# Optimization experiments

Hardware: AMD Instinct MI355X
Metric: run time of the kernel (lower is better)

Reference implementation:

```python
import jax, jax.numpy as jnp
import numpy as np

B = 65536
IN = 64
H = 16
PF = 64


def _linear_params(key, out_dim, in_dim):
    k1, k2 = jax.random.split(key)
    bound = 1.0 / np.sqrt(in_dim)
    W = jax.random.uniform(k1, (out_dim, in_dim), jnp.float32, -bound, bound)
    b = jax.random.uniform(k2, (out_dim,), jnp.float32, -bound, bound)
    return W, b


def setup_inputs() -> dict:
    key = jax.random.key(0)
    ks = jax.random.split(key, 20)
    inp = {}
    for i, name in enumerate(['a', 'v', 'l', 'p_a', 'p_v', 'p_l', 'mean']):
        inp[name] = jax.random.normal(ks[i], (B, IN), jnp.float32)
    inp['Wa'], inp['ba'] = _linear_params(ks[7], H, IN)
    inp['Wv'], inp['bv'] = _linear_params(ks[8], H, IN)
    inp['Wl'], inp['bl'] = _linear_params(ks[9], H, IN)
    inp['Wap'], inp['bap'] = _linear_params(ks[10], H, IN)
    inp['Wvp'], inp['bvp'] = _linear_params(ks[11], H, IN)
    inp['Wlp'], inp['blp'] = _linear_params(ks[12], H, IN)
    inp['Wf1'], inp['bf1'] = _linear_params(ks[13], PF, H ** 3 // 16)
    inp['Wfp1'], inp['bfp1'] = _linear_params(ks[14], PF, H ** 3 // 16)
    inp['Wng'], inp['bng'] = _linear_params(ks[15], 64, 128)
    inp['rm1'] = jnp.zeros((128,), jnp.float32)  # normGate2 running_mean buffers (eval mode)
    inp['rm2'] = jnp.zeros((128,), jnp.float32)
    return inp


def _maxpool2(x):
    # 2x2 stride-2 max pool over the last two dims of [B, Hd, Wd]
    b, hd, wd = x.shape
    return x.reshape(b, hd // 2, 2, wd // 2, 2).max(axis=(2, 4))


def _trimodal_fusion(x_h, y_h, z_h):
    # outer product [B,H,H] -> pool -> [B,H*H//4,1] bmm [B,1,H] -> pool -> flatten
    f = x_h[:, :, None] * y_h[:, None, :]            # [B,16,16]
    f = _maxpool2(f)                                 # [B,8,8]
    f = f.reshape(-1, H * H // 4, 1) * z_h[:, None, :]  # [B,64,16]
    f = _maxpool2(f)                                 # [B,32,8]
    return f.reshape(x_h.shape[0], -1)               # [B,256]


def _norm_gate(x, running_mean):
    # eval-mode normGate2: y = x * sigmoid(|x - running_mean|)
    return x * jax.nn.sigmoid(jnp.abs(x - running_mean))


def reference(a, v, l, p_a, p_v, p_l, mean,
              Wa, ba, Wv, bv, Wl, bl, Wap, bap, Wvp, bvp, Wlp, blp,
              Wf1, bf1, Wfp1, bfp1, Wng, bng, rm1, rm2):
    a_h = jax.nn.sigmoid(a @ Wa.T + ba)
    v_h = jax.nn.sigmoid(v @ Wv.T + bv)
    l_h = jax.nn.sigmoid(l @ Wl.T + bl)
    fusion_1 = jax.nn.leaky_relu(_trimodal_fusion(a_h, v_h, l_h) @ Wf1.T + bf1)

    pa_h = jax.nn.sigmoid(p_a @ Wap.T + bap)
    pv_h = jax.nn.sigmoid(p_v @ Wvp.T + bvp)
    pl_h = jax.nn.sigmoid(p_l @ Wlp.T + blp)
    fusion_2 = jax.nn.leaky_relu(_trimodal_fusion(pa_h, pv_h, pl_h) @ Wfp1.T + bfp1)

    out = _norm_gate(jnp.concatenate([fusion_2, mean], axis=1), rm1)   # [B,128]
    out = out @ Wng.T + bng                                            # [B,64]
    out = _norm_gate(jnp.concatenate([out, fusion_1], axis=1), rm2)    # [B,128]
    return out
```

## Files before the change

### kernel.cpp

```cpp
#include <hip/hip_runtime.h>
#include <hip/hip_bf16.h>


typedef __attribute__((ext_vector_type(8))) short short8;
typedef __attribute__((ext_vector_type(4))) float f32x4;

#define MFMA16(A, B, C) __builtin_amdgcn_mfma_f32_16x16x32_bf16((A), (B), (C), 0, 0, 0)

#define ASM_LOAD_F4(dst, p) \
    asm volatile("global_load_dwordx4 %0, %1, off" : "=v"(dst) : "v"(p) : "memory")
#define VMWAIT(N) do { asm volatile("s_waitcnt vmcnt(" #N ")" ::: "memory"); \
                       __builtin_amdgcn_sched_barrier(0); } while (0)

__device__ __forceinline__ float fast_sigmoid(float x) {
    return __builtin_amdgcn_rcpf(1.0f + __expf(-x));
}
__device__ __forceinline__ float gate(float x, float rm) {
    return x * fast_sigmoid(fabsf(x - rm));
}
__device__ __forceinline__ float lrelu(float x) {
    return x >= 0.0f ? x : 0.01f * x;
}
__device__ __forceinline__ short f2bf(float f) {
    union { float f; unsigned u; } x; x.f = f;
    unsigned r = (x.u + 0x7FFF + ((x.u >> 16) & 1)) >> 16;
    return (short)r;
}
__device__ __forceinline__ short8 pack8(const float* xs) {
    union { short8 s; __hip_bfloat162 h[4]; } u;
    #pragma unroll
    for (int i = 0; i < 4; ++i) {
        float2 t; t.x = xs[2 * i]; t.y = xs[2 * i + 1];
        u.h[i] = __float22bfloat162_rn(t);
    }
    return u.s;
}
__device__ __forceinline__ f32x4 pmax_xor(f32x4 v, int mask) {
    f32x4 r;
    #pragma unroll
    for (int i = 0; i < 4; ++i) r[i] = fmaxf(v[i], __shfl_xor(v[i], mask, 64));
    return r;
}

__device__ __forceinline__ void dma_1k(const short* src, short* dst_lds, int lane) {
    __builtin_amdgcn_global_load_lds(
        (const __attribute__((address_space(1))) unsigned int*)(const void*)(src + lane * 8),
        (__attribute__((address_space(3))) unsigned int*)(void*)(dst_lds),
        16, 0, 0);
}

__device__ __forceinline__ void proj_mfma2r(const f32x4* in,
                                            const short8* __restrict__ wfr,
                                            const float* __restrict__ bias,
                                            int lane, f32x4& h0, f32x4& h1) {
    const int m = lane & 15;
    f32x4 a0; a0[0] = a0[1] = a0[2] = a0[3] = 0.0f;
    f32x4 a1 = a0;
    #pragma unroll
    for (int t = 0; t < 2; ++t) {
        const short8 frag = wfr[t * 64 + lane];
        float xs0[8] = {in[2*t][0], in[2*t][1], in[2*t][2], in[2*t][3],
                        in[2*t+1][0], in[2*t+1][1], in[2*t+1][2], in[2*t+1][3]};
        float xs1[8] = {in[4+2*t][0], in[4+2*t][1], in[4+2*t][2], in[4+2*t][3],
                        in[4+2*t+1][0], in[4+2*t+1][1], in[4+2*t+1][2], in[4+2*t+1][3]};
        a0 = MFMA16(pack8(xs0), frag, a0);
        a1 = MFMA16(pack8(xs1), frag, a1);
    }
    const float bn = bias[m];
    #pragma unroll
    for (int r = 0; r < 4; ++r) {
        h0[r] = fast_sigmoid(a0[r] + bn);
        h1[r] = fast_sigmoid(a1[r] + bn);
    }
}

__device__ __forceinline__ void stage_pools(f32x4 hx, f32x4 hy, f32x4 hz, int lane,
                                            float* __restrict__ sX,
                                            float* __restrict__ sY,
                                            float* __restrict__ sZ) {
    const int quad = lane >> 4, ln = lane & 15;
    f32x4 X = pmax_xor(hx, 1);
    f32x4 Y = pmax_xor(pmax_xor(hy, 1), 2);
    f32x4 Z = pmax_xor(hz, 1);
    #pragma unroll
    for (int r = 0; r < 4; ++r) {
        const int sm = quad * 4 + r;
        sX[(ln >> 1) * 16 + sm] = X[r];
        sY[(ln >> 2) * 16 + sm] = Y[r];
        sZ[(ln >> 1) * 16 + sm] = Z[r];
    }
}

__device__ __forceinline__ void fusion_mfma2(const short8* __restrict__ wfr,
                                             const float* __restrict__ bias,
                                             const float* __restrict__ sP0,
                                             const float* __restrict__ sP1,
                                             int lane,
                                             f32x4 acc0[4], f32x4 acc1[4]) {
    const int m = lane & 15, quad = lane >> 4;
    const float* sX0 = sP0; const float* sY0 = sP0 + 128; const float* sZ0 = sP0 + 192;
    const float* sX1 = sP1; const float* sY1 = sP1 + 128; const float* sZ1 = sP1 + 192;
    #pragma unroll
    for (int nt = 0; nt < 4; ++nt) {
        const float bb = bias[nt * 16 + m];
        acc0[nt][0] = acc0[nt][1] = acc0[nt][2] = acc0[nt][3] = bb;
        acc1[nt][0] = acc1[nt][1] = acc1[nt][2] = acc1[nt][3] = bb;
    }
    float zr0[8], zr1[8], xr0[8], xr1[8];
    #pragma unroll
    for (int j = 0; j < 8; ++j) {
        zr0[j] = sZ0[j * 16 + m]; zr1[j] = sZ1[j * 16 + m];
        xr0[j] = sX0[j * 16 + m]; xr1[j] = sX1[j * 16 + m];
    }
    const float yq0 = sY0[quad * 16 + m];
    const float yq1 = sY1[quad * 16 + m];
    #pragma unroll
    for (int t = 0; t < 8; ++t) {
        const float xy0 = xr0[t] * yq0;
        const float xy1 = xr1[t] * yq1;
        float p0[8], p1[8];
        #pragma unroll
        for (int j = 0; j < 8; ++j) { p0[j] = xy0 * zr0[j]; p1[j] = xy1 * zr1[j]; }
        const short8 af0 = pack8(p0);
        const short8 af1 = pack8(p1);
        #pragma unroll
        for (int nt = 0; nt < 4; ++nt) {
            const short8 frag = wfr[(t * 4 + nt) * 64 + lane];
            acc0[nt] = MFMA16(af0, frag, acc0[nt]);
            acc1[nt] = MFMA16(af1, frag, acc1[nt]);
        }
    }
}

__global__ __launch_bounds__(256, 2)
void fused_fwd(const float* __restrict__ a,  const float* __restrict__ v,
               const float* __restrict__ l,  const float* __restrict__ pa,
               const float* __restrict__ pv, const float* __restrict__ pl,
               const float* __restrict__ mean,
               const short* __restrict__ ws, float* __restrict__ out) {
    __shared__ __align__(16) short sFrag[27648];
    __shared__ __align__(16) float sScr[4][1280];
    __shared__ __align__(16) float sBias[368];

    const int tid = threadIdx.x;
    const int lane = tid & 63;
    const int w = tid >> 6;
    const int m = lane & 15;
    const int quad = lane >> 4;
    const int p1 = blockIdx.x & 1;
    const int p  = blockIdx.x >> 1;

    {
        const int nU = p1 ? 38 : 54;
        for (int u = w; u < nU; u += 4) {
            const short* src;
            if (u < 6)       src = ws + (p1 ? 0 : 3072) + u * 512;
            else if (u < 38) src = ws + (p1 ? 6144 : 22528) + (u - 6) * 512;
            else             src = ws + 38912 + (u - 38) * 512;
            dma_1k(src, sFrag + u * 512, lane);
        }
        const float* wsF = (const float*)(ws + 47104);
        const int bOff = p1 ? 0 : 176;
        const int bCnt = p1 ? 176 : 368;
        for (int t = tid; t < bCnt; t += 256) sBias[t] = wsF[bOff + t];
    }
    __syncthreads();

    const short8* projT = (const short8*)sFrag;
    const short8* fusT  = (const short8*)(sFrag + 3072);
    const short8* ngT   = (const short8*)(sFrag + 19456);

    const float* bA = sBias;
    const float* bB = sBias + 16;
    const float* bC = sBias + 32;
    const float* bF = sBias + 48;
    const float* bNG  = sBias + 112;
    const float* RM1  = sBias + 176;
    const float* RM2A = sBias + 304;
    const float* RM2B = sBias + 112;

    float* sP0 = sScr[w];
    float* sP1 = sP0 + 320;
    short* sF0 = (short*)sScr[w];
    short* sF1 = sF0 + 1280;

    for (int c = 0; c < 2; ++c) {
        const int srow0 = (p * 2 + c) * 128 + w * 32;

        if (!p1) {
            f32x4 inA[8], inB[8], inC[8], inM[8];
            {
                const float* x0 = pa + (size_t)srow0 * 64;
                const float* x1 = pv + (size_t)srow0 * 64;
                const float* x2 = pl + (size_t)srow0 * 64;
                const float* x3 = mean + (size_t)srow0 * 64;
                #pragma unroll
                for (int i = 0; i < 8; ++i) {
                    const int tile = i >> 2, t = (i >> 1) & 1, hf = i & 1;
                    const size_t off = (size_t)(tile * 16 + m) * 64 + t * 32 + quad * 8 + hf * 4;
                    ASM_LOAD_F4(inA[i], x0 + off);
                }
                #pragma unroll
                for (int i = 0; i < 8; ++i) {
                    const int tile = i >> 2, t = (i >> 1) & 1, hf = i & 1;
                    const size_t off = (size_t)(tile * 16 + m) * 64 + t * 32 + quad * 8 + hf * 4;
                    ASM_LOAD_F4(inB[i], x1 + off);
                }
                #pragma unroll
                for (int i = 0; i < 8; ++i) {
                    const int tile = i >> 2, t = (i >> 1) & 1, hf = i & 1;
                    const size_t off = (size_t)(tile * 16 + m) * 64 + t * 32 + quad * 8 + hf * 4;
                    ASM_LOAD_F4(inC[i], x2 + off);
                }
                #pragma unroll
                for (int i = 0; i < 8; ++i) {
                    const int tile = i >> 2, t = (i >> 1) & 1, hf = i & 1;
                    const size_t off = (size_t)(tile * 16 + m) * 64 + t * 32 + quad * 8 + hf * 4;
                    ASM_LOAD_F4(inM[i], x3 + off);
                }
            }

            f32x4 hx0, hx1, hy0, hy1, hz0, hz1;
            VMWAIT(24);
            proj_mfma2r(inA, projT + 0 * 128, bA, lane, hx0, hx1);
            VMWAIT(16);
            proj_mfma2r(inB, projT + 1 * 128, bB, lane, hy0, hy1);
            VMWAIT(8);
            proj_mfma2r(inC, projT + 2 * 128, bC, lane, hz0, hz1);
            stage_pools(hx0, hy0, hz0, lane, sP0, sP0 + 128, sP0 + 192);
            stage_pools(hx1, hy1, hz1, lane, sP1, sP1 + 128, sP1 + 192);

            f32x4 f20[4], f21[4];
            fusion_mfma2(fusT, bF, sP0, sP1, lane, f20, f21);

            #pragma unroll
            for (int nt = 0; nt < 4; ++nt) {
                const float r1 = RM1[nt * 16 + m];
                #pragma unroll
                for (int r = 0; r < 4; ++r) {
                    sF0[(quad * 4 + r) * 80 + nt * 16 + m] = f2bf(gate(lrelu(f20[nt][r]), r1));
                    sF1[(quad * 4 + r) * 80 + nt * 16 + m] = f2bf(gate(lrelu(f21[nt][r]), r1));
                }
            }

            f32x4 h0[4], h1[4];
            #pragma unroll
            for (int nt = 0; nt < 4; ++nt) {
                const float bb = bNG[nt * 16 + m];
                h0[nt][0] = h0[nt][1] = h0[nt][2] = h0[nt][3] = bb;
                h1[nt][0] = h1[nt][1] = h1[nt][2] = h1[nt][3] = bb;
            }
            #pragma unroll
            for (int t = 0; t < 2; ++t) {
                const short8 af0 = *(const short8*)(sF0 + m * 80 + t * 32 + quad * 8);
                const short8 af1 = *(const short8*)(sF1 + m * 80 + t * 32 + quad * 8);
                #pragma unroll
                for (int nt = 0; nt < 4; ++nt) {
                    const short8 frag = ngT[(t * 4 + nt) * 64 + lane];
                    h0[nt] = MFMA16(af0, frag, h0[nt]);
                    h1[nt] = MFMA16(af1, frag, h1[nt]);
                }
            }
            VMWAIT(0);
            #pragma unroll
            for (int t2 = 0; t2 < 2; ++t2) {
                const f32x4 r0 = *(const f32x4*)(RM1 + 64 + t2 * 32 + quad * 8);
                const f32x4 r1 = *(const f32x4*)(RM1 + 64 + t2 * 32 + quad * 8 + 4);
                const f32x4 u0 = inM[2 * t2],     u1 = inM[2 * t2 + 1];
                const f32x4 w0 = inM[4 + 2 * t2], w1 = inM[4 + 2 * t2 + 1];
                float g0[8] = { gate(u0[0], r0[0]), gate(u0[1], r0[1]), gate(u0[2], r0[2]), gate(u0[3], r0[3]),
                                gate(u1[0], r1[0]), gate(u1[1], r1[1]), gate(u1[2], r1[2]), gate(u1[3], r1[3]) };
                float g1[8] = { gate(w0[0], r0[0]), gate(w0[1], r0[1]), gate(w0[2], r0[2]), gate(w0[3], r0[3]),
                                gate(w1[0], r1[0]), gate(w1[1], r1[1]), gate(w1[2], r1[2]), gate(w1[3], r1[3]) };
                const short8 af0 = pack8(g0);
                const short8 af1 = pack8(g1);
                #pragma unroll
                for (int nt = 0; nt < 4; ++nt) {
                    const short8 frag = ngT[((2 + t2) * 4 + nt) * 64 + lane];
                    h0[nt] = MFMA16(af0, frag, h0[nt]);
                    h1[nt] = MFMA16(af1, frag, h1[nt]);
                }
            }

            #pragma unroll
            for (int nt = 0; nt < 4; ++nt) {
                const float r2a = RM2A[nt * 16 + m];
                #pragma unroll
                for (int r = 0; r < 4; ++r) {
                    const size_t row0 = (size_t)(srow0 + quad * 4 + r) * 128;
                    const size_t row1 = (size_t)(srow0 + 16 + quad * 4 + r) * 128;
                    out[row0 + nt * 16 + m] = gate(h0[nt][r], r2a);
                    out[row1 + nt * 16 + m] = gate(h1[nt][r], r2a);
                }
            }
        } else {
            f32x4 inA[8], inB[8], inC[8];
            {
                const float* x0 = a + (size_t)srow0 * 64;
                const float* x1 = v + (size_t)srow0 * 64;
                const float* x2 = l + (size_t)srow0 * 64;
                #pragma unroll
                for (int i = 0; i < 8; ++i) {
                    const int tile = i >> 2, t = (i >> 1) & 1, hf = i & 1;
                    const size_t off = (size_t)(tile * 16 + m) * 64 + t * 32 + quad * 8 + hf * 4;
                    ASM_LOAD_F4(inA[i], x0 + off);
                }
                #pragma unroll
                for (int i = 0; i < 8; ++i) {
                    const int tile = i >> 2, t = (i >> 1) & 1, hf = i & 1;
                    const size_t off = (size_t)(tile * 16 + m) * 64 + t * 32 + quad * 8 + hf * 4;
                    ASM_LOAD_F4(inB[i], x1 + off);
                }
                #pragma unroll
                for (int i = 0; i < 8; ++i) {
                    const int tile = i >> 2, t = (i >> 1) & 1, hf = i & 1;
                    const size_t off = (size_t)(tile * 16 + m) * 64 + t * 32 + quad * 8 + hf * 4;
                    ASM_LOAD_F4(inC[i], x2 + off);
                }
            }

            f32x4 hx0, hx1, hy0, hy1, hz0, hz1;
            VMWAIT(16);
            proj_mfma2r(inA, projT + 0 * 128, bA, lane, hx0, hx1);
            VMWAIT(8);
            proj_mfma2r(inB, projT + 1 * 128, bB, lane, hy0, hy1);
            VMWAIT(0);
            proj_mfma2r(inC, projT + 2 * 128, bC, lane, hz0, hz1);
            stage_pools(hx0, hy0, hz0, lane, sP0, sP0 + 128, sP0 + 192);
            stage_pools(hx1, hy1, hz1, lane, sP1, sP1 + 128, sP1 + 192);

            f32x4 f10[4], f11[4];
            fusion_mfma2(fusT, bF, sP0, sP1, lane, f10, f11);

            #pragma unroll
            for (int nt = 0; nt < 4; ++nt) {
                const float r2b = RM2B[nt * 16 + m];
                #pragma unroll
                for (int r = 0; r < 4; ++r) {
                    const size_t row0 = (size_t)(srow0 + quad * 4 + r) * 128;
                    const size_t row1 = (size_t)(srow0 + 16 + quad * 4 + r) * 128;
                    out[row0 + 64 + nt * 16 + m] = gate(lrelu(f10[nt][r]), r2b);
                    out[row1 + 64 + nt * 16 + m] = gate(lrelu(f11[nt][r]), r2b);
                }
            }
        }
    }
}

__global__ void build_frags(const float* __restrict__ Wa,  const float* __restrict__ Wv,
                            const float* __restrict__ Wl,  const float* __restrict__ Wap,
                            const float* __restrict__ Wvp, const float* __restrict__ Wlp,
                            const float* __restrict__ Wf1, const float* __restrict__ Wfp1,
                            const float* __restrict__ Wng,
                            const float* __restrict__ ba,  const float* __restrict__ bv,
                            const float* __restrict__ bl,  const float* __restrict__ bap,
                            const float* __restrict__ bvp, const float* __restrict__ blp,
                            const float* __restrict__ bf1, const float* __restrict__ bfp1,
                            const float* __restrict__ bng, const float* __restrict__ rm1,
                            const float* __restrict__ rm2, short* __restrict__ ws) {
    const int i = blockIdx.x * 256 + threadIdx.x;
    if (i >= 47104 + 544) return;
    if (i >= 47104) {
        const int j = i - 47104;
        float fv;
        if (j < 176) {
            if (j < 16)       fv = ba[j];
            else if (j < 32)  fv = bv[j - 16];
            else if (j < 48)  fv = bl[j - 32];
            else if (j < 112) fv = bf1[j - 48];
            else              fv = rm2[64 + (j - 112)];
        } else {
            const int k = j - 176;
            if (k < 16)       fv = bap[k];
            else if (k < 32)  fv = bvp[k - 16];
            else if (k < 48)  fv = blp[k - 32];
            else if (k < 112) fv = bfp1[k - 48];
            else if (k < 176) fv = bng[k - 112];
            else if (k < 304) fv = rm1[k - 176];
            else              fv = rm2[k - 304];
        }
        ((float*)(ws + 47104))[j] = fv;
        return;
    }
    float val;
    if (i < 6144) {
        const float* W[6] = {Wa, Wv, Wl, Wap, Wvp, Wlp};
        const int mi = i >> 10, r = i & 1023;
        const int t = r >> 9, lane = (r >> 3) & 63, j = r & 7;
        val = W[mi][(lane & 15) * 64 + t * 32 + (lane >> 4) * 8 + j];
    } else if (i < 38912) {
        int r = i - 6144;
        const float* W = (r < 16384) ? Wf1 : Wfp1;
        r &= 16383;
        const int tn = r >> 9, lane = (r >> 3) & 63, j = r & 7;
        const int t = tn >> 2, nt = tn & 3;
        val = W[(nt * 16 + (lane & 15)) * 256 + t * 32 + (lane >> 4) * 8 + j];
    } else {
        const int r = i - 38912;
        const int tn = r >> 9, lane = (r >> 3) & 63, j = r & 7;
        const int t = tn >> 2, nt = tn & 3;
        val = Wng[(nt * 16 + (lane & 15)) * 128 + t * 32 + (lane >> 4) * 8 + j];
    }
    ws[i] = f2bf(val);
}

extern "C" void kernel_launch(void* const* d_in, const int* in_sizes, int n_in,
                              void* d_out, int out_size, void* d_ws, size_t ws_size,
                              hipStream_t stream) {
    const float* a    = (const float*)d_in[0];
    const float* v    = (const float*)d_in[1];
    const float* l    = (const float*)d_in[2];
    const float* pa   = (const float*)d_in[3];
    const float* pv   = (const float*)d_in[4];
    const float* pl   = (const float*)d_in[5];
    const float* mean = (const float*)d_in[6];
    const float* Wa   = (const float*)d_in[7];
    const float* ba   = (const float*)d_in[8];
    const float* Wv   = (const float*)d_in[9];
    const float* bv   = (const float*)d_in[10];
    const float* Wl   = (const float*)d_in[11];
    const float* bl   = (const float*)d_in[12];
    const float* Wap  = (const float*)d_in[13];
    const float* bap  = (const float*)d_in[14];
    const float* Wvp  = (const float*)d_in[15];
    const float* bvp  = (const float*)d_in[16];
    const float* Wlp  = (const float*)d_in[17];
    const float* blp  = (const float*)d_in[18];
    const float* Wf1  = (const float*)d_in[19];
    const float* bf1  = (const float*)d_in[20];
    const float* Wfp1 = (const float*)d_in[21];
    const float* bfp1 = (const float*)d_in[22];
    const float* Wng  = (const float*)d_in[23];
    const float* bng  = (const float*)d_in[24];
    const float* rm1  = (const float*)d_in[25];
    const float* rm2  = (const float*)d_in[26];

    short* ws = (short*)d_ws;

    build_frags<<<187, 256, 0, stream>>>(Wa, Wv, Wl, Wap, Wvp, Wlp,
                                         Wf1, Wfp1, Wng,
                                         ba, bv, bl, bap, bvp, blp,
                                         bf1, bfp1, bng, rm1, rm2, ws);
    fused_fwd<<<512, 256, 0, stream>>>(a, v, l, pa, pv, pl, mean,
                                       ws, (float*)d_out);
}
```

Measured before the change: 38.41 us.

## Software-pipeline global loads of second chunk behind first chunk's compute

Unrolls the two-chunk loop and issues the global loads for the second 128-row chunk while the first chunk's fusion and gate MFMAs are still running. The aim is to hide memory latency that the original per-chunk loop left exposed. In exchange, register pressure rises because two chunks of input fragments are live at once (launch bounds 256,2), which risks spills or lower occupancy. The vmcnt waits were retuned to match the new issue order.

```diff
diff --git a/kernel.cpp b/kernel.cpp
--- a/kernel.cpp
+++ b/kernel.cpp
@@ -47,6 +47,15 @@
         (const __attribute__((address_space(1))) unsigned int*)(const void*)(src + lane * 8),
         (__attribute__((address_space(3))) unsigned int*)(void*)(dst_lds),
         16, 0, 0);
+}
+
+__device__ __forceinline__ void issue8(f32x4* dst, const float* base, int m, int quad) {
+    #pragma unroll
+    for (int i = 0; i < 8; ++i) {
+        const int tile = i >> 2, t = (i >> 1) & 1, hf = i & 1;
+        const size_t off = (size_t)(tile * 16 + m) * 64 + t * 32 + quad * 8 + hf * 4;
+        ASM_LOAD_F4(dst[i], base + off);
+    }
 }
 
 __device__ __forceinline__ void proj_mfma2r(const f32x4* in,
@@ -150,6 +159,9 @@
     const int p1 = blockIdx.x & 1;
     const int p  = blockIdx.x >> 1;
 
+    const int s0 = (p * 2 + 0) * 128 + w * 32;
+    const int s1 = (p * 2 + 1) * 128 + w * 32;
+
     {
         const int nU = p1 ? 38 : 54;
         for (int u = w; u < nU; u += 4) {
@@ -184,49 +196,26 @@
     short* sF0 = (short*)sScr[w];
     short* sF1 = sF0 + 1280;
 
-    for (int c = 0; c < 2; ++c) {
-        const int srow0 = (p * 2 + c) * 128 + w * 32;
-
-        if (!p1) {
-            f32x4 inA[8], inB[8], inC[8], inM[8];
-            {
-                const float* x0 = pa + (size_t)srow0 * 64;
-                const float* x1 = pv + (size_t)srow0 * 64;
-                const float* x2 = pl + (size_t)srow0 * 64;
-                const float* x3 = mean + (size_t)srow0 * 64;
-                #pragma unroll
-                for (int i = 0; i < 8; ++i) {
-                    const int tile = i >> 2, t = (i >> 1) & 1, hf = i & 1;
-                    const size_t off = (size_t)(tile * 16 + m) * 64 + t * 32 + quad * 8 + hf * 4;
-                    ASM_LOAD_F4(inA[i], x0 + off);
-                }
-                #pragma unroll
-                for (int i = 0; i < 8; ++i) {
-                    const int tile = i >> 2, t = (i >> 1) & 1, hf = i & 1;
-                    const size_t off = (size_t)(tile * 16 + m) * 64 + t * 32 + quad * 8 + hf * 4;
-                    ASM_LOAD_F4(inB[i], x1 + off);
-                }
-                #pragma unroll
-                for (int i = 0; i < 8; ++i) {
-                    const int tile = i >> 2, t = (i >> 1) & 1, hf = i & 1;
-                    const size_t off = (size_t)(tile * 16 + m) * 64 + t * 32 + quad * 8 + hf * 4;
-                    ASM_LOAD_F4(inC[i], x2 + off);
-                }
-                #pragma unroll
-                for (int i = 0; i < 8; ++i) {
-                    const int tile = i >> 2, t = (i >> 1) & 1, hf = i & 1;
-                    const size_t off = (size_t)(tile * 16 + m) * 64 + t * 32 + quad * 8 + hf * 4;
-                    ASM_LOAD_F4(inM[i], x3 + off);
-                }
-            }
+    if (!p1) {
+        f32x4 A1[8], B1[8], C1[8], M1[8];
+        {
+            f32x4 A0[8], B0[8], C0[8], M0[8];
+            issue8(A0, pa + (size_t)s0 * 64, m, quad);
+            issue8(B0, pv + (size_t)s0 * 64, m, quad);
+            issue8(C0, pl + (size_t)s0 * 64, m, quad);
+            issue8(M0, mean + (size_t)s0 * 64, m, quad);
 
             f32x4 hx0, hx1, hy0, hy1, hz0, hz1;
             VMWAIT(24);
-            proj_mfma2r(inA, projT + 0 * 128, bA, lane, hx0, hx1);
+            proj_mfma2r(A0, projT + 0 * 128, bA, lane, hx0, hx1);
             VMWAIT(16);
-            proj_mfma2r(inB, projT + 1 * 128, bB, lane, hy0, hy1);
+            proj_mfma2r(B0, projT + 1 * 128, bB, lane, hy0, hy1);
             VMWAIT(8);
-            proj_mfma2r(inC, projT + 2 * 128, bC, lane, hz0, hz1);
+            proj_mfma2r(C0, projT + 2 * 128, bC, lane, hz0, hz1);
+            issue8(A1, pa + (size_t)s1 * 64, m, quad);
+            issue8(B1, pv + (size_t)s1 * 64, m, quad);
+            issue8(C1, pl + (size_t)s1 * 64, m, quad);
+
             stage_pools(hx0, hy0, hz0, lane, sP0, sP0 + 128, sP0 + 192);
             stage_pools(hx1, hy1, hz1, lane, sP1, sP1 + 128, sP1 + 192);
 
@@ -261,13 +250,13 @@
                     h1[nt] = MFMA16(af1, frag, h1[nt]);
                 }
             }
-            VMWAIT(0);
+            VMWAIT(24);
             #pragma unroll
             for (int t2 = 0; t2 < 2; ++t2) {
                 const f32x4 r0 = *(const f32x4*)(RM1 + 64 + t2 * 32 + quad * 8);
                 const f32x4 r1 = *(const f32x4*)(RM1 + 64 + t2 * 32 + quad * 8 + 4);
-                const f32x4 u0 = inM[2 * t2],     u1 = inM[2 * t2 + 1];
-                const f32x4 w0 = inM[4 + 2 * t2], w1 = inM[4 + 2 * t2 + 1];
+                const f32x4 u0 = M0[2 * t2],     u1 = M0[2 * t2 + 1];
+                const f32x4 w0 = M0[4 + 2 * t2], w1 = M0[4 + 2 * t2 + 1];
                 float g0[8] = { gate(u0[0], r0[0]), gate(u0[1], r0[1]), gate(u0[2], r0[2]), gate(u0[3], r0[3]),
                                 gate(u1[0], r1[0]), gate(u1[1], r1[1]), gate(u1[2], r1[2]), gate(u1[3], r1[3]) };
                 float g1[8] = { gate(w0[0], r0[0]), gate(w0[1], r0[1]), gate(w0[2], r0[2]), gate(w0[3], r0[3]),
@@ -281,51 +270,110 @@
                     h1[nt] = MFMA16(af1, frag, h1[nt]);
                 }
             }
-
+            issue8(M1, mean + (size_t)s1 * 64, m, quad);
             #pragma unroll
             for (int nt = 0; nt < 4; ++nt) {
                 const float r2a = RM2A[nt * 16 + m];
                 #pragma unroll
                 for (int r = 0; r < 4; ++r) {
-                    const size_t row0 = (size_t)(srow0 + quad * 4 + r) * 128;
-                    const size_t row1 = (size_t)(srow0 + 16 + quad * 4 + r) * 128;
+                    const size_t row0 = (size_t)(s0 + quad * 4 + r) * 128;
+                    const size_t row1 = (size_t)(s0 + 16 + quad * 4 + r) * 128;
                     out[row0 + nt * 16 + m] = gate(h0[nt][r], r2a);
                     out[row1 + nt * 16 + m] = gate(h1[nt][r], r2a);
                 }
             }
-        } else {
-            f32x4 inA[8], inB[8], inC[8];
-            {
-                const float* x0 = a + (size_t)srow0 * 64;
-                const float* x1 = v + (size_t)srow0 * 64;
-                const float* x2 = l + (size_t)srow0 * 64;
-                #pragma unroll
-                for (int i = 0; i < 8; ++i) {
-                    const int tile = i >> 2, t = (i >> 1) & 1, hf = i & 1;
-                    const size_t off = (size_t)(tile * 16 + m) * 64 + t * 32 + quad * 8 + hf * 4;
-                    ASM_LOAD_F4(inA[i], x0 + off);
-                }
-                #pragma unroll
-                for (int i = 0; i < 8; ++i) {
-                    const int tile = i >> 2, t = (i >> 1) & 1, hf = i & 1;
-                    const size_t off = (size_t)(tile * 16 + m) * 64 + t * 32 + quad * 8 + hf * 4;
-                    ASM_LOAD_F4(inB[i], x1 + off);
-                }
-                #pragma unroll
-                for (int i = 0; i < 8; ++i) {
-                    const int tile = i >> 2, t = (i >> 1) & 1, hf = i & 1;
-                    const size_t off = (size_t)(tile * 16 + m) * 64 + t * 32 + quad * 8 + hf * 4;
-                    ASM_LOAD_F4(inC[i], x2 + off);
-                }
-            }
+        }
+
+        VMWAIT(0);
+        {
+            f32x4 hx0, hx1, hy0, hy1, hz0, hz1;
+            proj_mfma2r(A1, projT + 0 * 128, bA, lane, hx0, hx1);
+            proj_mfma2r(B1, projT + 1 * 128, bB, lane, hy0, hy1);
+            proj_mfma2r(C1, projT + 2 * 128, bC, lane, hz0, hz1);
+            stage_pools(hx0, hy0, hz0, lane, sP0, sP0 + 128, sP0 + 192);
+            stage_pools(hx1, hy1, hz1, lane, sP1, sP1 + 128, sP1 + 192);
+
+            f32x4 f20[4], f21[4];
+            fusion_mfma2(fusT, bF, sP0, sP1, lane, f20, f21);
+
+            #pragma unroll
+            for (int nt = 0; nt < 4; ++nt) {
+                const float r1 = RM1[nt * 16 + m];
+                #pragma unroll
+                for (int r = 0; r < 4; ++r) {
+                    sF0[(quad * 4 + r) * 80 + nt * 16 + m] = f2bf(gate(lrelu(f20[nt][r]), r1));
+                    sF1[(quad * 4 + r) * 80 + nt * 16 + m] = f2bf(gate(lrelu(f21[nt][r]), r1));
+                }
+            }
+
+            f32x4 h0[4], h1[4];
+            #pragma unroll
+            for (int nt = 0; nt < 4; ++nt) {
+                const float bb = bNG[nt * 16 + m];
+                h0[nt][0] = h0[nt][1] = h0[nt][2] = h0[nt][3] = bb;
+                h1[nt][0] = h1[nt][1] = h1[nt][2] = h1[nt][3] = bb;
+            }
+            #pragma unroll
+            for (int t = 0; t < 2; ++t) {
+                const short8 af0 = *(const short8*)(sF0 + m * 80 + t * 32 + quad * 8);
+                const short8 af1 = *(const short8*)(sF1 + m * 80 + t * 32 + quad * 8);
+                #pragma unroll
+                for (int nt = 0; nt < 4; ++nt) {
+                    const short8 frag = ngT[(t * 4 + nt) * 64 + lane];
+                    h0[nt] = MFMA16(af0, frag, h0[nt]);
+                    h1[nt] = MFMA16(af1, frag, h1[nt]);
+                }
+            }
+            #pragma unroll
+            for (int t2 = 0; t2 < 2; ++t2) {
+                const f32x4 r0 = *(const f32x4*)(RM1 + 64 + t2 * 32 + quad * 8);
+                const f32x4 r1 = *(const f32x4*)(RM1 + 64 + t2 * 32 + quad * 8 + 4);
+                const f32x4 u0 = M1[2 * t2],     u1 = M1[2 * t2 + 1];
+                const f32x4 w0 = M1[4 + 2 * t2], w1 = M1[4 + 2 * t2 + 1];
+                float g0[8] = { gate(u0[0], r0[0]), gate(u0[1], r0[1]), gate(u0[2], r0[2]), gate(u0[3], r0[3]),
+                                gate(u1[0], r1[0]), gate(u1[1], r1[1]), gate(u1[2], r1[2]), gate(u1[3], r1[3]) };
+                float g1[8] = { gate(w0[0], r0[0]), gate(w0[1], r0[1]), gate(w0[2], r0[2]), gate(w0[3], r0[3]),
+                                gate(w1[0], r1[0]), gate(w1[1], r1[1]), gate(w1[2], r1[2]), gate(w1[3], r1[3]) };
+                const short8 af0 = pack8(g0);
+                const short8 af1 = pack8(g1);
+                #pragma unroll
+                for (int nt = 0; nt < 4; ++nt) {
+                    const short8 frag = ngT[((2 + t2) * 4 + nt) * 64 + lane];
+                    h0[nt] = MFMA16(af0, frag, h0[nt]);
+                    h1[nt] = MFMA16(af1, frag, h1[nt]);
+                }
+            }
+            #pragma unroll
+            for (int nt = 0; nt < 4; ++nt) {
+                const float r2a = RM2A[nt * 16 + m];
+                #pragma unroll
+                for (int r = 0; r < 4; ++r) {
+                    const size_t row0 = (size_t)(s1 + quad * 4 + r) * 128;
+                    const size_t row1 = (size_t)(s1 + 16 + quad * 4 + r) * 128;
+                    out[row0 + nt * 16 + m] = gate(h0[nt][r], r2a);
+                    out[row1 + nt * 16 + m] = gate(h1[nt][r], r2a);
+                }
+            }
+        }
+    } else {
+        f32x4 A1[8], B1[8], C1[8];
+        {
+            f32x4 A0[8], B0[8], C0[8];
+            issue8(A0, a + (size_t)s0 * 64, m, quad);
+            issue8(B0, v + (size_t)s0 * 64, m, quad);
+            issue8(C0, l + (size_t)s0 * 64, m, quad);
 
             f32x4 hx0, hx1, hy0, hy1, hz0, hz1;
             VMWAIT(16);
-            proj_mfma2r(inA, projT + 0 * 128, bA, lane, hx0, hx1);
+            proj_mfma2r(A0, projT + 0 * 128, bA, lane, hx0, hx1);
             VMWAIT(8);
-            proj_mfma2r(inB, projT + 1 * 128, bB, lane, hy0, hy1);
+            proj_mfma2r(B0, projT + 1 * 128, bB, lane, hy0, hy1);
             VMWAIT(0);
-            proj_mfma2r(inC, projT + 2 * 128, bC, lane, hz0, hz1);
+            proj_mfma2r(C0, projT + 2 * 128, bC, lane, hz0, hz1);
+            issue8(A1, a + (size_t)s1 * 64, m, quad);
+            issue8(B1, v + (size_t)s1 * 64, m, quad);
+            issue8(C1, l + (size_t)s1 * 64, m, quad);
+
             stage_pools(hx0, hy0, hz0, lane, sP0, sP0 + 128, sP0 + 192);
             stage_pools(hx1, hy1, hz1, lane, sP1, sP1 + 128, sP1 + 192);
 
@@ -337,8 +385,33 @@
                 const float r2b = RM2B[nt * 16 + m];
                 #pragma unroll
                 for (int r = 0; r < 4; ++r) {
-                    const size_t row0 = (size_t)(srow0 + quad * 4 + r) * 128;
-                    const size_t row1 = (size_t)(srow0 + 16 + quad * 4 + r) * 128;
+                    const size_t row0 = (size_t)(s0 + quad * 4 + r) * 128;
+                    const size_t row1 = (size_t)(s0 + 16 + quad * 4 + r) * 128;
+                    out[row0 + 64 + nt * 16 + m] = gate(lrelu(f10[nt][r]), r2b);
+                    out[row1 + 64 + nt * 16 + m] = gate(lrelu(f11[nt][r]), r2b);
+                }
+            }
+        }
+
+        VMWAIT(0);
+        {
+            f32x4 hx0, hx1, hy0, hy1, hz0, hz1;
+            proj_mfma2r(A1, projT + 0 * 128, bA, lane, hx0, hx1);
+            proj_mfma2r(B1, projT + 1 * 128, bB, lane, hy0, hy1);
+            proj_mfma2r(C1, projT + 2 * 128, bC, lane, hz0, hz1);
+            stage_pools(hx0, hy0, hz0, lane, sP0, sP0 + 128, sP0 + 192);
+            stage_pools(hx1, hy1, hz1, lane, sP1, sP1 + 128, sP1 + 192);
+
+            f32x4 f10[4], f11[4];
+            fusion_mfma2(fusT, bF, sP0, sP1, lane, f10, f11);
+
+            #pragma unroll
+            for (int nt = 0; nt < 4; ++nt) {
+                const float r2b = RM2B[nt * 16 + m];
+                #pragma unroll
+                for (int r = 0; r < 4; ++r) {
+                    const size_t row0 = (size_t)(s1 + quad * 4 + r) * 128;
+                    const size_t row1 = (size_t)(s1 + 16 + quad * 4 + r) * 128;
                     out[row0 + 64 + nt * 16 + m] = gate(lrelu(f10[nt][r]), r2b);
                     out[row1 + 64 + nt * 16 + m] = gate(lrelu(f11[nt][r]), r2b);
                 }
```

Measured after the change: 42.31 us. +10.2%, slower.
